# Optimization experiments

Measured on AMD Instinct MI355X. Metric: run time of the kernel, lower is better.

Reference implementation:

```python
import jax, jax.numpy as jnp
import numpy as np

GAMMA = 0.99
GAE_LAMBDA = 0.95
CLIP = 0.2
ENT_COEF = 0.01
VF_COEF = 0.5


def setup_inputs() -> dict:
    key = jax.random.key(0)
    ks = jax.random.split(key, 12)
    T, D, H, A = 65536, 512, 256, 16
    obs = jax.random.normal(ks[0], (T, D), dtype=jnp.float32)
    actions = jax.random.randint(ks[1], (T,), 0, A, dtype=jnp.int32)
    logprobs = jax.random.normal(ks[2], (T,), dtype=jnp.float32)
    rewards = jax.random.normal(ks[3], (T,), dtype=jnp.float32)
    terms = jax.random.uniform(ks[4], (T,), dtype=jnp.float32)
    values = jax.random.normal(ks[5], (T,), dtype=jnp.float32)
    # orthogonal-init-like scaling (std sqrt(2) for trunk, 0.01 actor, 1.0 critic)
    W1 = jax.random.normal(ks[6], (D, H), dtype=jnp.float32) * np.float32(np.sqrt(2.0 / D))
    b1 = jnp.zeros((H,), jnp.float32)
    W2 = jax.random.normal(ks[7], (H, H), dtype=jnp.float32) * np.float32(np.sqrt(2.0 / H))
    b2 = jnp.zeros((H,), jnp.float32)
    Wa = jax.random.normal(ks[8], (H, A), dtype=jnp.float32) * np.float32(0.01 / np.sqrt(H))
    ba = jnp.zeros((A,), jnp.float32)
    Wc = jax.random.normal(ks[9], (H, 1), dtype=jnp.float32) * np.float32(1.0 / np.sqrt(H))
    bc = jnp.zeros((1,), jnp.float32)
    return {"obs": obs, "actions": actions, "logprobs": logprobs, "rewards": rewards,
            "terms": terms, "values": values, "W1": W1, "b1": b1, "W2": W2, "b2": b2,
            "Wa": Wa, "ba": ba, "Wc": Wc, "bc": bc}


def reference(obs, actions, logprobs, rewards, terms, values,
              W1, b1, W2, b2, Wa, ba, Wc, bc):
    # ---- GAE (torch.no_grad in original -> stop_gradient) ----
    nonterm = 1.0 - terms                                   # [T]
    next_vals = jnp.concatenate([values[1:], jnp.zeros((1,), values.dtype)])
    delta = rewards + GAMMA * next_vals * nonterm - values  # [T]

    def step(carry, x):  # reverse recurrence a_t = d_t + g*l*nt_t * a_{t+1}
        d, nt = x
        g = d + GAMMA * GAE_LAMBDA * nt * carry
        return g, g

    _, adv = jax.lax.scan(step, jnp.float32(0.0), (delta, nonterm), reverse=True)
    adv = jax.lax.stop_gradient(adv)
    returns = adv + jax.lax.stop_gradient(values)
    vals_old = jax.lax.stop_gradient(values)

    # ---- actor-critic MLP (get_action_and_value) ----
    hidden = jnp.tanh(jnp.tanh(obs @ W1 + b1) @ W2 + b2)    # [T,256]
    logits = hidden @ Wa + ba                               # [T,A]
    logp = jax.nn.log_softmax(logits, axis=-1)
    newlp = jnp.take_along_axis(logp, actions[:, None].astype(jnp.int32), axis=1)[:, 0]
    entropy = -jnp.sum(jnp.exp(logp) * logp, axis=-1)       # [T]
    value = (hidden @ Wc + bc)[:, 0]                        # [T]

    # ---- clipped PPO losses (single full-batch minibatch) ----
    ratio = jnp.exp(newlp - logprobs)
    a = (adv - adv.mean()) / (adv.std() + 1e-8)
    pg_loss = jnp.maximum(-a * ratio, -a * jnp.clip(ratio, 1.0 - CLIP, 1.0 + CLIP)).mean()
    v_clipped = vals_old + jnp.clip(value - vals_old, -CLIP, CLIP)
    v_loss = 0.5 * jnp.maximum((value - returns) ** 2, (v_clipped - returns) ** 2).mean()
    loss = pg_loss - ENT_COEF * entropy.mean() + VF_COEF * v_loss
    return loss
```

## Files before the change

kernel.cpp:

```cpp
#include <hip/hip_runtime.h>


#define TT 65536

typedef float f32x4 __attribute__((ext_vector_type(4)));
typedef __bf16 bf16x8 __attribute__((ext_vector_type(8)));
typedef unsigned short u16x8 __attribute__((ext_vector_type(8)));
typedef unsigned short u16x4 __attribute__((ext_vector_type(4)));

__device__ __forceinline__ unsigned short f2bf(float f) {
    unsigned int u = __float_as_uint(f);
    unsigned int r = (u + 0x7fffu + ((u >> 16) & 1u)) >> 16;
    return (unsigned short)r;
}

__device__ __forceinline__ float fast_tanh(float x) {
    float e = __expf(2.0f * x);
    return fmaf(-2.0f, __builtin_amdgcn_rcpf(e + 1.0f), 1.0f);
}

__device__ __forceinline__ void async_lds16(void* lds, const void* g) {
    __builtin_amdgcn_global_load_lds(
        (const __attribute__((address_space(1))) unsigned int*)g,
        (__attribute__((address_space(3))) unsigned int*)lds, 16, 0, 0);
}

__device__ __forceinline__ void suffix_scan256(float* sC, float* sD, int i) {
    float c = sC[i], d = sD[i];
#pragma unroll
    for (int s = 1; s < 256; s <<= 1) {
        float c2 = 1.0f, d2 = 0.0f;
        if (i + s < 256) { c2 = sC[i + s]; d2 = sD[i + s]; }
        __syncthreads();
        d = d + c * d2;
        c = c * c2;
        sC[i] = c; sD[i] = d;
        __syncthreads();
    }
}

__device__ __forceinline__ void gae_cd(const float* rewards, const float* terms,
                                       const float* values, int t, float* c, float* d) {
    float nt = 1.0f - terms[t];
    float nv = (t + 1 < TT) ? values[t + 1] : 0.0f;
    *d = rewards[t] + 0.99f * nv * nt - values[t];
    *c = 0.99f * 0.95f * nt;
}

__global__ void k_prep_gae1(const float* __restrict__ W1, const float* __restrict__ W2,
                            const float* __restrict__ Wa, const float* __restrict__ Wc,
                            unsigned short* __restrict__ W1T, unsigned short* __restrict__ W2T,
                            unsigned short* __restrict__ WavT,
                            const float* __restrict__ rewards, const float* __restrict__ terms,
                            const float* __restrict__ values, float* __restrict__ aggC,
                            float* __restrict__ aggD) {
    if (blockIdx.x < 800) {
        int idx = blockIdx.x * 256 + threadIdx.x;
        if (idx < 131072) {
            int kt = idx >> 13;
            int L = (idx & 8191) >> 3, e = idx & 7;
            int row = L >> 2, p = L & 3;
            int k = kt * 32 + (((p ^ ((row >> 1) & 3)) << 3) | e);
            W1T[idx] = f2bf(W1[k * 256 + row]);
        } else if (idx < 196608) {
            int i = idx - 131072;
            int kt = i >> 13;
            int L = (i & 8191) >> 3, e = i & 7;
            int row = L >> 2, p = L & 3;
            int k = kt * 32 + (((p ^ ((row >> 1) & 3)) << 3) | e);
            W2T[i] = f2bf(W2[k * 256 + row]);
        } else if (idx < 204800) {
            int i = idx - 196608;
            int L = i >> 3, e = i & 7;
            int row = L >> 5, ec = (L & 31) << 3;
            int k = ((ec ^ ((row & 7) << 3)) | e);
            float v = (row < 16) ? Wa[k * 16 + row] : ((row == 16) ? Wc[k] : 0.0f);
            WavT[i] = f2bf(v);
        }
        return;
    }
    __shared__ float sC[256], sD[256];
    int i = threadIdx.x;
    int b = blockIdx.x - 800;
    int t = b * 256 + i;
    float c, d;
    gae_cd(rewards, terms, values, t, &c, &d);
    sC[i] = c; sD[i] = d;
    __syncthreads();
    suffix_scan256(sC, sD, i);
    if (i == 0) { aggC[b] = sC[0]; aggD[b] = sD[0]; }
}

__global__ void k_gae3(const float* __restrict__ rewards, const float* __restrict__ terms,
                       const float* __restrict__ values, const float* __restrict__ aggC,
                       const float* __restrict__ aggD, float* __restrict__ adv,
                       float* __restrict__ ret, float* __restrict__ sumP) {
    __shared__ float sC[256], sD[256];
    int i = threadIdx.x, b = blockIdx.x;
    sC[i] = aggC[i]; sD[i] = aggD[i];
    __syncthreads();
    suffix_scan256(sC, sD, i);
    float carry = (b < 255) ? sD[b + 1] : 0.0f;
    __syncthreads();

    int t = b * 256 + i;
    float c, d;
    gae_cd(rewards, terms, values, t, &c, &d);
    sC[i] = c; sD[i] = d;
    __syncthreads();
    suffix_scan256(sC, sD, i);
    float a = sD[i] + sC[i] * carry;
    adv[t] = a;
    ret[t] = a + values[t];
    __syncthreads();
    sC[i] = a; sD[i] = a * a;
    __syncthreads();
#pragma unroll
    for (int s = 128; s > 0; s >>= 1) {
        if (i < s) { sC[i] += sC[i + s]; sD[i] += sD[i + s]; }
        __syncthreads();
    }
    if (i == 0) { sumP[2 * b] = sC[0]; sumP[2 * b + 1] = sD[0]; }
}

__global__ __launch_bounds__(256, 3) void k_mlp(
    const float* __restrict__ obs, const int* __restrict__ actions,
    const float* __restrict__ logprobs, const float* __restrict__ values,
    const float* __restrict__ b1, const float* __restrict__ b2,
    const float* __restrict__ ba, const float* __restrict__ bc,
    const unsigned short* __restrict__ W1T, const unsigned short* __restrict__ W2T,
    const unsigned short* __restrict__ WavT, const float* __restrict__ adv,
    const float* __restrict__ ret, const float* __restrict__ sumP,
    float* __restrict__ lossP) {
    __shared__ __align__(16) unsigned char SM[53248];
    unsigned short* smB = (unsigned short*)SM;
    unsigned short* smA = (unsigned short*)(SM + 16384);
    unsigned short* smH = (unsigned short*)(SM + 20480);
    float* red = (float*)(SM + 20480);
    float* red2 = (float*)(SM + 16384);

    const int tid = threadIdx.x;
    const int wid = tid >> 6;
    const int lane = tid & 63;
    const int cl = lane & 15;
    const int gg = lane >> 4;
    const int bm0 = blockIdx.x * 64;

    const int arow = tid >> 2;
    const int aslot = tid & 3;
    const int adst = arow * 32 + ((aslot ^ ((arow >> 1) & 3)) << 3);
    const float* aSrc = obs + (size_t)(bm0 + arow) * 512 + aslot * 8;

    float meanA, rstdA;
    {
        red[tid] = sumP[2 * tid];
        red[256 + tid] = sumP[2 * tid + 1];
        __syncthreads();
#pragma unroll
        for (int s = 128; s > 0; s >>= 1) {
            if (tid < s) { red[tid] += red[tid + s]; red[256 + tid] += red[256 + tid + s]; }
            __syncthreads();
        }
        meanA = red[0] * (1.0f / TT);
        float var = red[256] * (1.0f / TT) - meanA * meanA;
        rstdA = 1.0f / (sqrtf(fmaxf(var, 0.0f)) + 1e-8f);
        __syncthreads();
    }

    float b1v[4], b2v[4];
#pragma unroll
    for (int n = 0; n < 4; ++n) {
        int c = wid * 64 + n * 16 + cl;
        b1v[n] = b1[c];
        b2v[n] = b2[c];
    }
    const float bav = ba[cl];
    const float bc0 = bc[0];

    f32x4 acc[4][4];
#pragma unroll
    for (int m = 0; m < 4; ++m)
#pragma unroll
        for (int n = 0; n < 4; ++n) acc[m][n] = (f32x4){0.f, 0.f, 0.f, 0.f};

    for (int t = 0; t < 16; ++t) {
        {
            const unsigned short* bsrc = W1T + t * 8192 + lane * 8;
#pragma unroll
            for (int c = 0; c < 4; ++c) {
                int chunk = wid * 4 + c;
                async_lds16(&smB[chunk * 512], bsrc + chunk * 512);
            }
            float4 a0 = *(const float4*)(aSrc + t * 32);
            float4 a1 = *(const float4*)(aSrc + t * 32 + 4);
            u16x8 cc;
            cc[0] = f2bf(a0.x); cc[1] = f2bf(a0.y); cc[2] = f2bf(a0.z); cc[3] = f2bf(a0.w);
            cc[4] = f2bf(a1.x); cc[5] = f2bf(a1.y); cc[6] = f2bf(a1.z); cc[7] = f2bf(a1.w);
            *(u16x8*)&smA[adst] = cc;
        }
        __syncthreads();
        bf16x8 av[4], bv[4];
#pragma unroll
        for (int m = 0; m < 4; ++m) {
            int ra = m * 16 + cl;
            av[m] = *(const bf16x8*)&smA[ra * 32 + ((gg ^ ((ra >> 1) & 3)) << 3)];
        }
#pragma unroll
        for (int n = 0; n < 4; ++n) {
            int rb = wid * 64 + n * 16 + cl;
            bv[n] = *(const bf16x8*)&smB[rb * 32 + ((gg ^ ((rb >> 1) & 3)) << 3)];
        }
#pragma unroll
        for (int m = 0; m < 4; ++m)
#pragma unroll
            for (int n = 0; n < 4; ++n)
                acc[m][n] = __builtin_amdgcn_mfma_f32_16x16x32_bf16(av[m], bv[n], acc[m][n], 0, 0, 0);
        __syncthreads();
    }

#pragma unroll
    for (int m = 0; m < 4; ++m)
#pragma unroll
        for (int n = 0; n < 4; ++n)
#pragma unroll
            for (int j = 0; j < 4; ++j) {
                int r = m * 16 + gg * 4 + j;
                int c = wid * 64 + n * 16 + cl;
                smH[r * 256 + (c ^ ((r & 7) << 3))] = f2bf(fast_tanh(acc[m][n][j] + b1v[n]));
                acc[m][n][j] = 0.0f;
            }
    __syncthreads();

    for (int t = 0; t < 8; ++t) {
        {
            const unsigned short* bsrc = W2T + t * 8192 + lane * 8;
#pragma unroll
            for (int c = 0; c < 4; ++c) {
                int chunk = wid * 4 + c;
                async_lds16(&smB[chunk * 512], bsrc + chunk * 512);
            }
        }
        __syncthreads();
        bf16x8 av[4], bv[4];
#pragma unroll
        for (int m = 0; m < 4; ++m) {
            int ra = m * 16 + cl;
            av[m] = *(const bf16x8*)&smH[ra * 256 + ((t * 32 + gg * 8) ^ ((ra & 7) << 3))];
        }
#pragma unroll
        for (int n = 0; n < 4; ++n) {
            int rb = wid * 64 + n * 16 + cl;
            bv[n] = *(const bf16x8*)&smB[rb * 32 + ((gg ^ ((rb >> 1) & 3)) << 3)];
        }
#pragma unroll
        for (int m = 0; m < 4; ++m)
#pragma unroll
            for (int n = 0; n < 4; ++n)
                acc[m][n] = __builtin_amdgcn_mfma_f32_16x16x32_bf16(av[m], bv[n], acc[m][n], 0, 0, 0);
        __syncthreads();
    }

    {
        const unsigned short* bsrc = WavT + lane * 8;
#pragma unroll
        for (int c = 0; c < 4; ++c) {
            int chunk = wid * 4 + c;
            async_lds16(&smB[chunk * 512], bsrc + chunk * 512);
        }
    }
#pragma unroll
    for (int m = 0; m < 4; ++m)
#pragma unroll
        for (int n = 0; n < 4; ++n)
#pragma unroll
            for (int j = 0; j < 4; ++j) {
                int r = m * 16 + gg * 4 + j;
                int c = wid * 64 + n * 16 + cl;
                smH[r * 256 + (c ^ ((r & 7) << 3))] = f2bf(fast_tanh(acc[m][n][j] + b2v[n]));
            }
    __syncthreads();

    float lsum = 0.0f;
    {
        f32x4 acc_a = {0.f, 0.f, 0.f, 0.f}, acc_v = {0.f, 0.f, 0.f, 0.f};
#pragma unroll
        for (int kk = 0; kk < 8; ++kk) {
            int r = wid * 16 + cl;
            bf16x8 av = *(const bf16x8*)&smH[r * 256 + ((kk * 32 + gg * 8) ^ ((r & 7) << 3))];
            int ra2 = cl;
            bf16x8 bva = *(const bf16x8*)&smB[ra2 * 256 + ((kk * 32 + gg * 8) ^ ((ra2 & 7) << 3))];
            int rv = 16 + cl;
            bf16x8 bvv = *(const bf16x8*)&smB[rv * 256 + ((kk * 32 + gg * 8) ^ ((rv & 7) << 3))];
            acc_a = __builtin_amdgcn_mfma_f32_16x16x32_bf16(av, bva, acc_a, 0, 0, 0);
            acc_v = __builtin_amdgcn_mfma_f32_16x16x32_bf16(av, bvv, acc_v, 0, 0, 0);
        }

        const int t0 = bm0 + wid * 16;
#pragma unroll
        for (int j = 0; j < 4; ++j) {
            int t = t0 + gg * 4 + j;
            float lg = acc_a[j] + bav;
            float mx = lg;
#pragma unroll
            for (int dd = 1; dd < 16; dd <<= 1) mx = fmaxf(mx, __shfl_xor(mx, dd));
            float ex = __expf(lg - mx);
            float se = ex;
#pragma unroll
            for (int dd = 1; dd < 16; dd <<= 1) se += __shfl_xor(se, dd);
            float ls = __logf(se);
            float lp = lg - mx - ls;
            float pl = __expf(lp) * lp;
            float ent = pl;
#pragma unroll
            for (int dd = 1; dd < 16; dd <<= 1) ent += __shfl_xor(ent, dd);
            ent = -ent;
            int act = actions[t];
            float newlp = __shfl(lp, (lane & 48) | act);
            float val = __shfl(acc_v[j], lane & 48) + bc0;

            float lpo = logprobs[t];
            float at = (adv[t] - meanA) * rstdA;
            float rt = ret[t];
            float vo = values[t];
            float ratio = __expf(newlp - lpo);
            float rcl = fminf(fmaxf(ratio, 0.8f), 1.2f);
            float pg = fmaxf(-at * ratio, -at * rcl);
            float vcl = vo + fminf(fmaxf(val - vo, -0.2f), 0.2f);
            float dv = val - rt, dvc = vcl - rt;
            float vl = fmaxf(dv * dv, dvc * dvc);
            if (cl == 0) lsum += pg - 0.01f * ent + 0.25f * vl;
        }
        lsum += __shfl_xor(lsum, 16);
        lsum += __shfl_xor(lsum, 32);
    }
    __syncthreads();
    if (lane == 0) red2[wid] = lsum;
    __syncthreads();
    if (tid == 0) lossP[blockIdx.x] = red2[0] + red2[1] + red2[2] + red2[3];
}

__global__ void k_final(const float* __restrict__ lossP, float* __restrict__ out) {
    __shared__ float s[256];
    int i = threadIdx.x;
    s[i] = lossP[i] + lossP[i + 256] + lossP[i + 512] + lossP[i + 768];
    __syncthreads();
#pragma unroll
    for (int st = 128; st > 0; st >>= 1) {
        if (i < st) s[i] += s[i + st];
        __syncthreads();
    }
    if (i == 0) out[0] = s[0] * (1.0f / TT);
}

extern "C" void kernel_launch(void* const* d_in, const int* in_sizes, int n_in,
                              void* d_out, int out_size, void* d_ws, size_t ws_size,
                              hipStream_t stream) {
    const float* obs      = (const float*)d_in[0];
    const int*   actions  = (const int*)d_in[1];
    const float* logprobs = (const float*)d_in[2];
    const float* rewards  = (const float*)d_in[3];
    const float* terms    = (const float*)d_in[4];
    const float* values   = (const float*)d_in[5];
    const float* W1 = (const float*)d_in[6];
    const float* b1 = (const float*)d_in[7];
    const float* W2 = (const float*)d_in[8];
    const float* b2 = (const float*)d_in[9];
    const float* Wa = (const float*)d_in[10];
    const float* ba = (const float*)d_in[11];
    const float* Wc = (const float*)d_in[12];
    const float* bc = (const float*)d_in[13];

    char* ws = (char*)d_ws;
    unsigned short* W1T  = (unsigned short*)(ws + 0);
    unsigned short* W2T  = (unsigned short*)(ws + 262144);
    unsigned short* WavT = (unsigned short*)(ws + 393216);
    float* advp  = (float*)(ws + 409600);
    float* retp  = (float*)(ws + 671744);
    float* aggC  = (float*)(ws + 933888);
    float* aggD  = (float*)(ws + 934912);
    float* sumP  = (float*)(ws + 936960);
    float* lossP = (float*)(ws + 939072);

    k_prep_gae1<<<1056, 256, 0, stream>>>(W1, W2, Wa, Wc, W1T, W2T, WavT,
                                          rewards, terms, values, aggC, aggD);
    k_gae3<<<256, 256, 0, stream>>>(rewards, terms, values, aggC, aggD, advp, retp, sumP);
    k_mlp<<<1024, 256, 0, stream>>>(obs, actions, logprobs, values, b1, b2, ba, bc,
                                    W1T, W2T, WavT, advp, retp, sumP, lossP);
    k_final<<<1, 256, 0, stream>>>(lossP, (float*)d_out);
}
```

Before: 80.01 us.

## Double-buffer layer-1 GEMM tiles and hoist advantage stats into separate kernel

The first-layer GEMM loop now double-buffers both the obs tile and the W1 tile in LDS. It prefetches the next step's global data while MFMAs run on the current step, which removes one barrier per iteration. The W2 tile prefetch is moved to after compute, and bf16 conversion now uses the packed v_cvt_pk_bf16_f32 instruction. The per-block reduction of the advantage mean/std partials is moved into a new single-block kernel, so each of the 1024 MLP blocks no longer repeats it, at the cost of an extra launch. LDS shrinks to 48KB by aliasing the hidden buffer with the first-layer B buffers.

```diff
diff --git a/kernel.cpp b/kernel.cpp
--- a/kernel.cpp
+++ b/kernel.cpp
@@ -6,12 +6,18 @@
 typedef float f32x4 __attribute__((ext_vector_type(4)));
 typedef __bf16 bf16x8 __attribute__((ext_vector_type(8)));
 typedef unsigned short u16x8 __attribute__((ext_vector_type(8)));
-typedef unsigned short u16x4 __attribute__((ext_vector_type(4)));
+typedef unsigned int u32x4 __attribute__((ext_vector_type(4)));
 
 __device__ __forceinline__ unsigned short f2bf(float f) {
     unsigned int u = __float_as_uint(f);
     unsigned int r = (u + 0x7fffu + ((u >> 16) & 1u)) >> 16;
     return (unsigned short)r;
+}
+
+__device__ __forceinline__ unsigned int cvt_pk_bf16(float a, float b) {
+    unsigned int r;
+    asm volatile("v_cvt_pk_bf16_f32 %0, %1, %2" : "=v"(r) : "v"(a), "v"(b));
+    return r;
 }
 
 __device__ __forceinline__ float fast_tanh(float x) {
@@ -123,6 +129,24 @@
     if (i == 0) { sumP[2 * b] = sC[0]; sumP[2 * b + 1] = sD[0]; }
 }
 
+__global__ void k_gae4(const float* __restrict__ sumP, float* __restrict__ stats) {
+    __shared__ float s1[256], s2[256];
+    int i = threadIdx.x;
+    s1[i] = sumP[2 * i]; s2[i] = sumP[2 * i + 1];
+    __syncthreads();
+#pragma unroll
+    for (int s = 128; s > 0; s >>= 1) {
+        if (i < s) { s1[i] += s1[i + s]; s2[i] += s2[i + s]; }
+        __syncthreads();
+    }
+    if (i == 0) {
+        float mean = s1[0] * (1.0f / TT);
+        float var = s2[0] * (1.0f / TT) - mean * mean;
+        stats[0] = mean;
+        stats[1] = 1.0f / (sqrtf(fmaxf(var, 0.0f)) + 1e-8f);
+    }
+}
+
 __global__ __launch_bounds__(256, 3) void k_mlp(
     const float* __restrict__ obs, const int* __restrict__ actions,
     const float* __restrict__ logprobs, const float* __restrict__ values,
@@ -130,14 +154,13 @@
     const float* __restrict__ ba, const float* __restrict__ bc,
     const unsigned short* __restrict__ W1T, const unsigned short* __restrict__ W2T,
     const unsigned short* __restrict__ WavT, const float* __restrict__ adv,
-    const float* __restrict__ ret, const float* __restrict__ sumP,
+    const float* __restrict__ ret, const float* __restrict__ stats,
     float* __restrict__ lossP) {
-    __shared__ __align__(16) unsigned char SM[53248];
-    unsigned short* smB = (unsigned short*)SM;
-    unsigned short* smA = (unsigned short*)(SM + 16384);
-    unsigned short* smH = (unsigned short*)(SM + 20480);
-    float* red = (float*)(SM + 20480);
-    float* red2 = (float*)(SM + 16384);
+    __shared__ __align__(16) unsigned char SM[49152];
+    unsigned short* smB1 = (unsigned short*)SM;
+    unsigned short* smA  = (unsigned short*)(SM + 32768);
+    unsigned short* smH  = (unsigned short*)SM;
+    unsigned short* smB2 = (unsigned short*)(SM + 32768);
 
     const int tid = threadIdx.x;
     const int wid = tid >> 6;
@@ -151,21 +174,7 @@
     const int adst = arow * 32 + ((aslot ^ ((arow >> 1) & 3)) << 3);
     const float* aSrc = obs + (size_t)(bm0 + arow) * 512 + aslot * 8;
 
-    float meanA, rstdA;
-    {
-        red[tid] = sumP[2 * tid];
-        red[256 + tid] = sumP[2 * tid + 1];
-        __syncthreads();
-#pragma unroll
-        for (int s = 128; s > 0; s >>= 1) {
-            if (tid < s) { red[tid] += red[tid + s]; red[256 + tid] += red[256 + tid + s]; }
-            __syncthreads();
-        }
-        meanA = red[0] * (1.0f / TT);
-        float var = red[256] * (1.0f / TT) - meanA * meanA;
-        rstdA = 1.0f / (sqrtf(fmaxf(var, 0.0f)) + 1e-8f);
-        __syncthreads();
-    }
+    const float meanA = stats[0], rstdA = stats[1];
 
     float b1v[4], b2v[4];
 #pragma unroll
@@ -183,64 +192,78 @@
 #pragma unroll
         for (int n = 0; n < 4; ++n) acc[m][n] = (f32x4){0.f, 0.f, 0.f, 0.f};
 
-    for (int t = 0; t < 16; ++t) {
-        {
-            const unsigned short* bsrc = W1T + t * 8192 + lane * 8;
-#pragma unroll
-            for (int c = 0; c < 4; ++c) {
-                int chunk = wid * 4 + c;
-                async_lds16(&smB[chunk * 512], bsrc + chunk * 512);
+    auto stageTile = [&](const unsigned short* src, unsigned short* dst) {
+#pragma unroll
+        for (int c = 0; c < 4; ++c) {
+            int chunk = wid * 4 + c;
+            async_lds16(dst + chunk * 512, src + chunk * 512 + lane * 8);
+        }
+    };
+    auto cvtWriteA = [&](const float4& f0, const float4& f1, int buf) {
+        u32x4 pk;
+        pk[0] = cvt_pk_bf16(f0.x, f0.y);
+        pk[1] = cvt_pk_bf16(f0.z, f0.w);
+        pk[2] = cvt_pk_bf16(f1.x, f1.y);
+        pk[3] = cvt_pk_bf16(f1.z, f1.w);
+        *(u32x4*)&smA[buf * 2048 + adst] = pk;
+    };
+
+    {
+        float4 a0 = *(const float4*)(aSrc);
+        float4 a1 = *(const float4*)(aSrc + 4);
+        stageTile(W1T, smB1);
+        cvtWriteA(a0, a1, 0);
+        __syncthreads();
+#pragma unroll
+        for (int t = 0; t < 16; ++t) {
+            if (t < 15) {
+                a0 = *(const float4*)(aSrc + (t + 1) * 32);
+                a1 = *(const float4*)(aSrc + (t + 1) * 32 + 4);
+                stageTile(W1T + (t + 1) * 8192, smB1 + ((t + 1) & 1) * 8192);
             }
-            float4 a0 = *(const float4*)(aSrc + t * 32);
-            float4 a1 = *(const float4*)(aSrc + t * 32 + 4);
-            u16x8 cc;
-            cc[0] = f2bf(a0.x); cc[1] = f2bf(a0.y); cc[2] = f2bf(a0.z); cc[3] = f2bf(a0.w);
-            cc[4] = f2bf(a1.x); cc[5] = f2bf(a1.y); cc[6] = f2bf(a1.z); cc[7] = f2bf(a1.w);
-            *(u16x8*)&smA[adst] = cc;
-        }
-        __syncthreads();
-        bf16x8 av[4], bv[4];
-#pragma unroll
-        for (int m = 0; m < 4; ++m) {
-            int ra = m * 16 + cl;
-            av[m] = *(const bf16x8*)&smA[ra * 32 + ((gg ^ ((ra >> 1) & 3)) << 3)];
-        }
-#pragma unroll
-        for (int n = 0; n < 4; ++n) {
-            int rb = wid * 64 + n * 16 + cl;
-            bv[n] = *(const bf16x8*)&smB[rb * 32 + ((gg ^ ((rb >> 1) & 3)) << 3)];
-        }
-#pragma unroll
-        for (int m = 0; m < 4; ++m)
-#pragma unroll
-            for (int n = 0; n < 4; ++n)
-                acc[m][n] = __builtin_amdgcn_mfma_f32_16x16x32_bf16(av[m], bv[n], acc[m][n], 0, 0, 0);
-        __syncthreads();
-    }
-
+            bf16x8 av[4], bv[4];
+#pragma unroll
+            for (int m = 0; m < 4; ++m) {
+                int ra = m * 16 + cl;
+                av[m] = *(const bf16x8*)&smA[(t & 1) * 2048 + ra * 32 + ((gg ^ ((ra >> 1) & 3)) << 3)];
+            }
+#pragma unroll
+            for (int n = 0; n < 4; ++n) {
+                int rb = wid * 64 + n * 16 + cl;
+                bv[n] = *(const bf16x8*)&smB1[(t & 1) * 8192 + rb * 32 + ((gg ^ ((rb >> 1) & 3)) << 3)];
+            }
+#pragma unroll
+            for (int m = 0; m < 4; ++m)
+#pragma unroll
+                for (int n = 0; n < 4; ++n)
+                    acc[m][n] = __builtin_amdgcn_mfma_f32_16x16x32_bf16(av[m], bv[n], acc[m][n], 0, 0, 0);
+            if (t < 15) cvtWriteA(a0, a1, (t + 1) & 1);
+            __syncthreads();
+        }
+    }
+
+    stageTile(W2T, smB2);
 #pragma unroll
     for (int m = 0; m < 4; ++m)
 #pragma unroll
         for (int n = 0; n < 4; ++n)
 #pragma unroll
-            for (int j = 0; j < 4; ++j) {
-                int r = m * 16 + gg * 4 + j;
+            for (int jp = 0; jp < 2; ++jp) {
+                float v0 = fast_tanh(acc[m][n][2 * jp] + b1v[n]);
+                float v1 = fast_tanh(acc[m][n][2 * jp + 1] + b1v[n]);
+                unsigned int p = cvt_pk_bf16(v0, v1);
+                int r0 = m * 16 + gg * 4 + 2 * jp;
                 int c = wid * 64 + n * 16 + cl;
-                smH[r * 256 + (c ^ ((r & 7) << 3))] = f2bf(fast_tanh(acc[m][n][j] + b1v[n]));
-                acc[m][n][j] = 0.0f;
+                smH[r0 * 256 + (c ^ ((r0 & 7) << 3))] = (unsigned short)p;
+                int r1 = r0 + 1;
+                smH[r1 * 256 + (c ^ ((r1 & 7) << 3))] = (unsigned short)(p >> 16);
+                acc[m][n][2 * jp] = 0.0f;
+                acc[m][n][2 * jp + 1] = 0.0f;
             }
     __syncthreads();
 
+#pragma unroll
     for (int t = 0; t < 8; ++t) {
-        {
-            const unsigned short* bsrc = W2T + t * 8192 + lane * 8;
-#pragma unroll
-            for (int c = 0; c < 4; ++c) {
-                int chunk = wid * 4 + c;
-                async_lds16(&smB[chunk * 512], bsrc + chunk * 512);
-            }
-        }
-        __syncthreads();
         bf16x8 av[4], bv[4];
 #pragma unroll
         for (int m = 0; m < 4; ++m) {
@@ -250,7 +273,7 @@
 #pragma unroll
         for (int n = 0; n < 4; ++n) {
             int rb = wid * 64 + n * 16 + cl;
-            bv[n] = *(const bf16x8*)&smB[rb * 32 + ((gg ^ ((rb >> 1) & 3)) << 3)];
+            bv[n] = *(const bf16x8*)&smB2[rb * 32 + ((gg ^ ((rb >> 1) & 3)) << 3)];
         }
 #pragma unroll
         for (int m = 0; m < 4; ++m)
@@ -258,25 +281,25 @@
             for (int n = 0; n < 4; ++n)
                 acc[m][n] = __builtin_amdgcn_mfma_f32_16x16x32_bf16(av[m], bv[n], acc[m][n], 0, 0, 0);
         __syncthreads();
-    }
-
-    {
-        const unsigned short* bsrc = WavT + lane * 8;
-#pragma unroll
-        for (int c = 0; c < 4; ++c) {
-            int chunk = wid * 4 + c;
-            async_lds16(&smB[chunk * 512], bsrc + chunk * 512);
-        }
-    }
+        if (t < 7) stageTile(W2T + (t + 1) * 8192, smB2);
+        else       stageTile(WavT, smB2);
+        __syncthreads();
+    }
+
 #pragma unroll
     for (int m = 0; m < 4; ++m)
 #pragma unroll
         for (int n = 0; n < 4; ++n)
 #pragma unroll
-            for (int j = 0; j < 4; ++j) {
-                int r = m * 16 + gg * 4 + j;
+            for (int jp = 0; jp < 2; ++jp) {
+                float v0 = fast_tanh(acc[m][n][2 * jp] + b2v[n]);
+                float v1 = fast_tanh(acc[m][n][2 * jp + 1] + b2v[n]);
+                unsigned int p = cvt_pk_bf16(v0, v1);
+                int r0 = m * 16 + gg * 4 + 2 * jp;
                 int c = wid * 64 + n * 16 + cl;
-                smH[r * 256 + (c ^ ((r & 7) << 3))] = f2bf(fast_tanh(acc[m][n][j] + b2v[n]));
+                smH[r0 * 256 + (c ^ ((r0 & 7) << 3))] = (unsigned short)p;
+                int r1 = r0 + 1;
+                smH[r1 * 256 + (c ^ ((r1 & 7) << 3))] = (unsigned short)(p >> 16);
             }
     __syncthreads();
 
@@ -288,9 +311,9 @@
             int r = wid * 16 + cl;
             bf16x8 av = *(const bf16x8*)&smH[r * 256 + ((kk * 32 + gg * 8) ^ ((r & 7) << 3))];
             int ra2 = cl;
-            bf16x8 bva = *(const bf16x8*)&smB[ra2 * 256 + ((kk * 32 + gg * 8) ^ ((ra2 & 7) << 3))];
+            bf16x8 bva = *(const bf16x8*)&smB2[ra2 * 256 + ((kk * 32 + gg * 8) ^ ((ra2 & 7) << 3))];
             int rv = 16 + cl;
-            bf16x8 bvv = *(const bf16x8*)&smB[rv * 256 + ((kk * 32 + gg * 8) ^ ((rv & 7) << 3))];
+            bf16x8 bvv = *(const bf16x8*)&smB2[rv * 256 + ((kk * 32 + gg * 8) ^ ((rv & 7) << 3))];
             acc_a = __builtin_amdgcn_mfma_f32_16x16x32_bf16(av, bva, acc_a, 0, 0, 0);
             acc_v = __builtin_amdgcn_mfma_f32_16x16x32_bf16(av, bvv, acc_v, 0, 0, 0);
         }
@@ -334,6 +357,7 @@
         lsum += __shfl_xor(lsum, 32);
     }
     __syncthreads();
+    float* red2 = (float*)SM;
     if (lane == 0) red2[wid] = lsum;
     __syncthreads();
     if (tid == 0) lossP[blockIdx.x] = red2[0] + red2[1] + red2[2] + red2[3];
@@ -379,12 +403,14 @@
     float* aggC  = (float*)(ws + 933888);
     float* aggD  = (float*)(ws + 934912);
     float* sumP  = (float*)(ws + 936960);
+    float* stats = (float*)(ws + 939008);
     float* lossP = (float*)(ws + 939072);
 
     k_prep_gae1<<<1056, 256, 0, stream>>>(W1, W2, Wa, Wc, W1T, W2T, WavT,
                                           rewards, terms, values, aggC, aggD);
     k_gae3<<<256, 256, 0, stream>>>(rewards, terms, values, aggC, aggD, advp, retp, sumP);
+    k_gae4<<<1, 256, 0, stream>>>(sumP, stats);
     k_mlp<<<1024, 256, 0, stream>>>(obs, actions, logprobs, values, b1, b2, ba, bc,
-                                    W1T, W2T, WavT, advp, retp, sumP, lossP);
+                                    W1T, W2T, WavT, advp, retp, stats, lossP);
     k_final<<<1, 256, 0, stream>>>(lossP, (float*)d_out);
 }
```

New measurement: 75.87 us. 1.05x faster.
